# Kernel optimization log

Hardware: AMD Instinct MI355X
Metric: run time of the kernel (lower is better)

Reference implementation:

```python
import jax, jax.numpy as jnp
import numpy as np

T, B, H, L = 1024, 64, 512, 2


def setup_inputs() -> dict:
    key = jax.random.key(0)
    ks = jax.random.split(key, 5)
    s = 1.0 / np.sqrt(H)
    return {
        "x": jax.random.normal(ks[0], (T, B, H), jnp.float32),
        "h0": jnp.zeros((L, B, H), jnp.float32),
        "c0": jnp.zeros((L, B, H), jnp.float32),
        "W_ih": jax.random.uniform(ks[1], (L, 4 * H, H), jnp.float32, -s, s),
        "W_hh": jax.random.uniform(ks[2], (L, 4 * H, H), jnp.float32, -s, s),
        "b_ih": jax.random.uniform(ks[3], (L, 4 * H), jnp.float32, -s, s),
        "b_hh": jax.random.uniform(ks[4], (L, 4 * H), jnp.float32, -s, s),
    }


def _run_layer(x, h0, c0, W_ih, W_hh, b_ih, b_hh):
    # Precompute input-to-gate projections for all timesteps: [T, B, 4H]
    x_gates = jnp.einsum('tbi,gi->tbg', x, W_ih) + b_ih + b_hh

    def step(carry, xg):
        h, c = carry
        gates = xg + h @ W_hh.T  # [B, 4H]
        i, f, g, o = jnp.split(gates, 4, axis=-1)
        i = jax.nn.sigmoid(i)
        f = jax.nn.sigmoid(f)
        g = jnp.tanh(g)
        o = jax.nn.sigmoid(o)
        c_next = f * c + i * g
        h_next = o * jnp.tanh(c_next)
        return (h_next, c_next), h_next

    (h_n, c_n), out = jax.lax.scan(step, (h0, c0), x_gates)
    return out, h_n, c_n


def reference(x, h0, c0, W_ih, W_hh, b_ih, b_hh):
    h_ns, c_ns = [], []
    layer_out = x
    for l in range(L):
        layer_out, h_n, c_n = _run_layer(
            layer_out, h0[l], c0[l], W_ih[l], W_hh[l], b_ih[l], b_hh[l])
        h_ns.append(h_n)
        c_ns.append(c_n)
    return layer_out, jnp.stack(h_ns, 0), jnp.stack(c_ns, 0)
```

## Files before the change

kernel.cpp:

```cpp
#include <hip/hip_runtime.h>
#include <math.h>

#define TT 1024
#define BB 64
#define HH 512
#define G4 2048
#define NBLK 256
#define NTHR 1024
#define KH (HH * BB)

#define HN_OFF ((size_t)TT * BB * HH)
#define CN_OFF (HN_OFF + (size_t)2 * BB * HH)

__device__ inline float sigm(float v) {
    return 1.0f / (1.0f + __expf(-v));
}
__device__ inline float tanh_fast(float v) {
    const float e = __expf(2.0f * v);
    return 1.0f - 2.0f / (e + 1.0f);
}

__device__ inline void store_coh(float* p, float v) {
    __hip_atomic_store(p, v, __ATOMIC_RELAXED, __HIP_MEMORY_SCOPE_AGENT);
}

extern "C" __global__ void __launch_bounds__(256)
xpose(const float* __restrict__ x, float* __restrict__ xT)
{
    __shared__ float tile[64][65];
    const int t   = blockIdx.x;
    const int kc  = blockIdx.y << 6;
    const int tid = threadIdx.x;

    const int kk = tid & 63;
    const int b0 = tid >> 6;
    const float* xp = x + (size_t)t * BB * HH;
    #pragma unroll
    for (int i = 0; i < 16; ++i) {
        const int b = b0 + (i << 2);
        tile[b][kk] = xp[(size_t)b * HH + kc + kk];
    }
    __syncthreads();
    const int b  = tid & 63;
    const int k0 = tid >> 6;
    float* xo = xT + (size_t)t * KH + (size_t)kc * BB;
    #pragma unroll
    for (int i = 0; i < 16; ++i) {
        const int kl = k0 + (i << 2);
        xo[kl * BB + b] = tile[b][kl];
    }
}

__device__ inline void grid_barrier(unsigned* gbar, unsigned* groot,
                                    unsigned barIdx, int bid)
{
    __syncthreads();
    if (threadIdx.x == 0) {
        const int g = bid & 15;
        const unsigned old = __hip_atomic_fetch_add(
            &gbar[g * 16], 1u, __ATOMIC_RELAXED, __HIP_MEMORY_SCOPE_AGENT);
        if (old == barIdx * 16u + 15u) {
            __hip_atomic_fetch_add(groot, 1u, __ATOMIC_RELAXED,
                                   __HIP_MEMORY_SCOPE_AGENT);
        }
        const unsigned tgt = (barIdx + 1u) * 16u;
        while (__hip_atomic_load(groot, __ATOMIC_RELAXED,
                                 __HIP_MEMORY_SCOPE_AGENT) < tgt) {
            __builtin_amdgcn_s_sleep(1);
        }
        __builtin_amdgcn_fence(__ATOMIC_ACQUIRE, "agent");
    }
    __syncthreads();
}

extern "C" __global__ void __launch_bounds__(NTHR)
lstm_scan(const float* __restrict__ h0,
          const float* __restrict__ c0,
          const float* __restrict__ Wih,
          const float* __restrict__ Whh,
          const float* __restrict__ bih,
          const float* __restrict__ bhh,
          const float* __restrict__ xT,
          float* __restrict__ out,
          float* __restrict__ h0buf,
          float* __restrict__ h1buf,
          unsigned* __restrict__ gbar,
          unsigned* __restrict__ groot)
{
    __shared__ float red[16][8][64];
    __shared__ __align__(16) float wlds[16][8][128];

    const int tid  = threadIdx.x;
    const int lane = tid & 63;
    const int w    = __builtin_amdgcn_readfirstlane(tid >> 6);
    const int bid  = blockIdx.x;
    const int hk0  = bid << 1;

    const int kbase = (w & 3) << 7;
    const int grp   = w >> 2;

    const float* Wbase;
    if      (grp == 0) Wbase = Wih;
    else if (grp == 1) Wbase = Whh;
    else if (grp == 2) Wbase = Wih + (size_t)G4 * HH;
    else               Wbase = Whh + (size_t)G4 * HH;

    #pragma unroll
    for (int rr = 0; rr < 8; ++rr) {
        const int row = ((rr >> 1) << 9) + hk0 + (rr & 1);
        const float* src = Wbase + (size_t)row * HH + kbase;
        wlds[w][rr][lane]      = src[lane];
        wlds[w][rr][lane + 64] = src[lane + 64];
    }

    float creg[2] = {0.f, 0.f};
    float bs[8];
    if (w == 0) {
        #pragma unroll
        for (int u = 0; u < 2; ++u) {
            const int hk = hk0 + u;
            store_coh(&h0buf[hk * BB + lane], h0[(size_t)lane * HH + hk]);
            creg[u] = c0[(size_t)lane * HH + hk];
        }
        #pragma unroll
        for (int rr = 0; rr < 8; ++rr) {
            const int row = ((rr >> 1) << 9) + hk0 + (rr & 1);
            bs[rr] = bih[row] + bhh[row];
        }
    } else if (w == 1) {
        #pragma unroll
        for (int u = 0; u < 2; ++u) {
            const int hk = hk0 + u;
            store_coh(&h1buf[hk * BB + lane], h0[(size_t)(BB + lane) * HH + hk]);
            creg[u] = c0[(size_t)(BB + lane) * HH + hk];
        }
        #pragma unroll
        for (int rr = 0; rr < 8; ++rr) {
            const int row = ((rr >> 1) << 9) + hk0 + (rr & 1);
            bs[rr] = bih[G4 + row] + bhh[G4 + row];
        }
    }

    unsigned barIdx = 0;
    grid_barrier(gbar, groot, barIdx, bid); ++barIdx;

    const float* wl = &wlds[w][0][0];

    for (int s = 0; s <= TT; ++s) {
        const float* act;
        if (grp == 0) {
            const int t0 = (s < TT) ? s : (TT - 1);
            act = xT + (size_t)t0 * KH + (size_t)kbase * BB;
        } else if (grp <= 2) {
            act = h0buf + (size_t)(s & 1) * KH + (size_t)kbase * BB;
        } else {
            act = h1buf + (size_t)((s + 1) & 1) * KH + (size_t)kbase * BB;
        }

        float acc[8];
        #pragma unroll
        for (int rr = 0; rr < 8; ++rr) acc[rr] = 0.0f;

        #pragma unroll 2
        for (int j = 0; j < 128; j += 4) {
            const float a0 = act[(j + 0) * BB + lane];
            const float a1 = act[(j + 1) * BB + lane];
            const float a2 = act[(j + 2) * BB + lane];
            const float a3 = act[(j + 3) * BB + lane];
            #pragma unroll
            for (int rr = 0; rr < 8; ++rr) {
                const float4 wv = *(const float4*)(wl + rr * 128 + j);
                acc[rr] = fmaf(a3, wv.w,
                           fmaf(a2, wv.z,
                            fmaf(a1, wv.y,
                             fmaf(a0, wv.x, acc[rr]))));
            }
        }

        #pragma unroll
        for (int rr = 0; rr < 8; ++rr) red[w][rr][lane] = acc[rr];
        __syncthreads();

        if (w == 0) {
            if (s < TT) {
                float g[8];
                #pragma unroll
                for (int rr = 0; rr < 8; ++rr) {
                    float t = red[0][rr][lane] + red[1][rr][lane]
                            + red[2][rr][lane] + red[3][rr][lane]
                            + red[4][rr][lane] + red[5][rr][lane]
                            + red[6][rr][lane] + red[7][rr][lane];
                    g[rr] = bs[rr] + t;
                }
                #pragma unroll
                for (int u = 0; u < 2; ++u) {
                    const float ig = sigm(g[0 + u]);
                    const float fg = sigm(g[2 + u]);
                    const float gg = tanh_fast(g[4 + u]);
                    const float og = sigm(g[6 + u]);
                    const float cn = fg * creg[u] + ig * gg;
                    const float hn = og * tanh_fast(cn);
                    creg[u] = cn;
                    const int hk = hk0 + u;
                    store_coh(&h0buf[(size_t)((s + 1) & 1) * KH + hk * BB + lane], hn);
                    if (s == TT - 1) {
                        out[HN_OFF + (size_t)lane * HH + hk] = hn;
                        out[CN_OFF + (size_t)lane * HH + hk] = cn;
                    }
                }
            }
        } else if (w == 1) {
            if (s >= 1) {
                const int t1 = s - 1;
                float g[8];
                #pragma unroll
                for (int rr = 0; rr < 8; ++rr) {
                    float t = red[8][rr][lane]  + red[9][rr][lane]
                            + red[10][rr][lane] + red[11][rr][lane]
                            + red[12][rr][lane] + red[13][rr][lane]
                            + red[14][rr][lane] + red[15][rr][lane];
                    g[rr] = bs[rr] + t;
                }
                #pragma unroll
                for (int u = 0; u < 2; ++u) {
                    const float ig = sigm(g[0 + u]);
                    const float fg = sigm(g[2 + u]);
                    const float gg = tanh_fast(g[4 + u]);
                    const float og = sigm(g[6 + u]);
                    const float cn = fg * creg[u] + ig * gg;
                    const float hn = og * tanh_fast(cn);
                    creg[u] = cn;
                    const int hk = hk0 + u;
                    store_coh(&h1buf[(size_t)(s & 1) * KH + hk * BB + lane], hn);
                    out[(size_t)t1 * BB * HH + (size_t)lane * HH + hk] = hn;
                    if (t1 == TT - 1) {
                        out[HN_OFF + (size_t)(BB + lane) * HH + hk] = hn;
                        out[CN_OFF + (size_t)(BB + lane) * HH + hk] = cn;
                    }
                }
            }
        }
        grid_barrier(gbar, groot, barIdx, bid); ++barIdx;
    }
}

extern "C" void kernel_launch(void* const* d_in, const int* in_sizes, int n_in,
                              void* d_out, int out_size, void* d_ws, size_t ws_size,
                              hipStream_t stream)
{
    (void)in_sizes; (void)n_in; (void)out_size; (void)ws_size;
    const float* x   = (const float*)d_in[0];
    const float* h0  = (const float*)d_in[1];
    const float* c0  = (const float*)d_in[2];
    const float* Wih = (const float*)d_in[3];
    const float* Whh = (const float*)d_in[4];
    const float* bih = (const float*)d_in[5];
    const float* bhh = (const float*)d_in[6];
    float* out = (float*)d_out;

    float* xT    = (float*)d_ws;
    float* h0buf = xT + (size_t)TT * KH;
    float* h1buf = h0buf + (size_t)2 * KH;
    unsigned* gbar  = (unsigned*)(h1buf + (size_t)2 * KH);
    unsigned* groot = gbar + 256;

    hipMemsetAsync(gbar, 0, (256 + 64) * sizeof(unsigned), stream);

    xpose<<<dim3(TT, 8), 256, 0, stream>>>(x, xT);

    void* args[] = {(void*)&h0, (void*)&c0, (void*)&Wih, (void*)&Whh,
                    (void*)&bih, (void*)&bhh, (void*)&xT, (void*)&out,
                    (void*)&h0buf, (void*)&h1buf, (void*)&gbar, (void*)&groot};
    hipLaunchCooperativeKernel((void*)lstm_scan, dim3(NBLK), dim3(NTHR),
                               args, 0, stream);
}
```

Measured before the change: 17.70 ms.

## Retile inner dot product to packed 2-wide FMAs over batch pairs

Each lane now handles two batch columns and four gate rows instead of one batch column and eight rows. Activations are loaded as float2 and accumulated with packed 2-wide FMAs, which halves the LDS weight reads per FMA and enables packed FP32 math. It also remaps block IDs to spread hidden units across XCDs, adds an occupancy hint to launch bounds, and vectorizes the layer-1 output stores to float2. Risks are higher register pressure and changed cache locality from the new block mapping.

After: 21.61 ms. 22.1% more time.

```diff
diff --git a/kernel.cpp b/kernel.cpp
--- a/kernel.cpp
+++ b/kernel.cpp
@@ -11,6 +11,8 @@
 
 #define HN_OFF ((size_t)TT * BB * HH)
 #define CN_OFF (HN_OFF + (size_t)2 * BB * HH)
+
+typedef float v2f __attribute__((ext_vector_type(2)));
 
 __device__ inline float sigm(float v) {
     return 1.0f / (1.0f + __expf(-v));
@@ -73,7 +75,7 @@
     __syncthreads();
 }
 
-extern "C" __global__ void __launch_bounds__(NTHR)
+extern "C" __global__ void __launch_bounds__(NTHR, 4)
 lstm_scan(const float* __restrict__ h0,
           const float* __restrict__ c0,
           const float* __restrict__ Wih,
@@ -87,17 +89,21 @@
           unsigned* __restrict__ gbar,
           unsigned* __restrict__ groot)
 {
-    __shared__ float red[16][8][64];
+    __shared__ __align__(16) float red[16][8][64];
     __shared__ __align__(16) float wlds[16][8][128];
 
     const int tid  = threadIdx.x;
     const int lane = tid & 63;
     const int w    = __builtin_amdgcn_readfirstlane(tid >> 6);
     const int bid  = blockIdx.x;
-    const int hk0  = bid << 1;
+    const int vb   = ((bid & 7) << 5) | (bid >> 3);
+    const int hk0  = vb << 1;
 
     const int kbase = (w & 3) << 7;
     const int grp   = w >> 2;
+
+    const int rg = lane >> 5;
+    const int b0 = (lane & 31) << 1;
 
     const float* Wbase;
     if      (grp == 0) Wbase = Wih;
@@ -144,7 +150,7 @@
     unsigned barIdx = 0;
     grid_barrier(gbar, groot, barIdx, bid); ++barIdx;
 
-    const float* wl = &wlds[w][0][0];
+    const float* wl = &wlds[w][rg << 2][0];
 
     for (int s = 0; s <= TT; ++s) {
         const float* act;
@@ -156,29 +162,36 @@
         } else {
             act = h1buf + (size_t)((s + 1) & 1) * KH + (size_t)kbase * BB;
         }
-
-        float acc[8];
-        #pragma unroll
-        for (int rr = 0; rr < 8; ++rr) acc[rr] = 0.0f;
+        const float* actp = act + b0;
+
+        v2f acc2[4];
+        #pragma unroll
+        for (int q = 0; q < 4; ++q) acc2[q] = (v2f){0.f, 0.f};
 
         #pragma unroll 2
         for (int j = 0; j < 128; j += 4) {
-            const float a0 = act[(j + 0) * BB + lane];
-            const float a1 = act[(j + 1) * BB + lane];
-            const float a2 = act[(j + 2) * BB + lane];
-            const float a3 = act[(j + 3) * BB + lane];
+            const v2f a0 = *(const v2f*)(actp + (j + 0) * BB);
+            const v2f a1 = *(const v2f*)(actp + (j + 1) * BB);
+            const v2f a2 = *(const v2f*)(actp + (j + 2) * BB);
+            const v2f a3 = *(const v2f*)(actp + (j + 3) * BB);
             #pragma unroll
-            for (int rr = 0; rr < 8; ++rr) {
-                const float4 wv = *(const float4*)(wl + rr * 128 + j);
-                acc[rr] = fmaf(a3, wv.w,
-                           fmaf(a2, wv.z,
-                            fmaf(a1, wv.y,
-                             fmaf(a0, wv.x, acc[rr]))));
+            for (int q = 0; q < 4; ++q) {
+                const float4 wv = *(const float4*)(wl + q * 128 + j);
+                const v2f w0 = {wv.x, wv.x};
+                const v2f w1 = {wv.y, wv.y};
+                const v2f w2 = {wv.z, wv.z};
+                const v2f w3 = {wv.w, wv.w};
+                acc2[q] = __builtin_elementwise_fma(a0, w0, acc2[q]);
+                acc2[q] = __builtin_elementwise_fma(a1, w1, acc2[q]);
+                acc2[q] = __builtin_elementwise_fma(a2, w2, acc2[q]);
+                acc2[q] = __builtin_elementwise_fma(a3, w3, acc2[q]);
             }
         }
 
         #pragma unroll
-        for (int rr = 0; rr < 8; ++rr) red[w][rr][lane] = acc[rr];
+        for (int q = 0; q < 4; ++q) {
+            *(v2f*)&red[w][(rg << 2) + q][b0] = acc2[q];
+        }
         __syncthreads();
 
         if (w == 0) {
@@ -221,6 +234,7 @@
                             + red[14][rr][lane] + red[15][rr][lane];
                     g[rr] = bs[rr] + t;
                 }
+                float hn2[2], cn2[2];
                 #pragma unroll
                 for (int u = 0; u < 2; ++u) {
                     const float ig = sigm(g[0 + u]);
@@ -230,13 +244,17 @@
                     const float cn = fg * creg[u] + ig * gg;
                     const float hn = og * tanh_fast(cn);
                     creg[u] = cn;
+                    cn2[u] = cn; hn2[u] = hn;
                     const int hk = hk0 + u;
                     store_coh(&h1buf[(size_t)(s & 1) * KH + hk * BB + lane], hn);
-                    out[(size_t)t1 * BB * HH + (size_t)lane * HH + hk] = hn;
-                    if (t1 == TT - 1) {
-                        out[HN_OFF + (size_t)(BB + lane) * HH + hk] = hn;
-                        out[CN_OFF + (size_t)(BB + lane) * HH + hk] = cn;
-                    }
+                }
+                *(float2*)&out[(size_t)t1 * BB * HH + (size_t)lane * HH + hk0] =
+                    make_float2(hn2[0], hn2[1]);
+                if (t1 == TT - 1) {
+                    *(float2*)&out[HN_OFF + (size_t)(BB + lane) * HH + hk0] =
+                        make_float2(hn2[0], hn2[1]);
+                    *(float2*)&out[CN_OFF + (size_t)(BB + lane) * HH + hk0] =
+                        make_float2(cn2[0], cn2[1]);
                 }
             }
         }
```

## Use packed FMA accumulators, remap block IDs across XCDs, vectorize output stores

Applied to the files above, without the earlier changes.

Rewrites the inner dot-product to use 2-wide vector FMAs, so the compiler can emit packed FP32 FMA (v_pk_fma_f32) with two partial sums per row that are added at the end. It also permutes the block-to-hidden-unit mapping so that consecutive hidden pairs land on blocks spread over the XCDs, which may change L2 locality of the h buffers. Output h/c stores for the two hidden units are merged into float2 writes. Together these aim to cut FMA issue count and scattered store transactions inside the latency-bound recurrent loop. The changed summation order perturbs floating-point results slightly.

After: 14.99 ms. 15.3% less time.

```diff
diff --git a/kernel.cpp b/kernel.cpp
--- a/kernel.cpp
+++ b/kernel.cpp
@@ -11,6 +11,8 @@
 
 #define HN_OFF ((size_t)TT * BB * HH)
 #define CN_OFF (HN_OFF + (size_t)2 * BB * HH)
+
+typedef float v2f __attribute__((ext_vector_type(2)));
 
 __device__ inline float sigm(float v) {
     return 1.0f / (1.0f + __expf(-v));
@@ -87,14 +89,15 @@
           unsigned* __restrict__ gbar,
           unsigned* __restrict__ groot)
 {
-    __shared__ float red[16][8][64];
+    __shared__ __align__(16) float red[16][8][64];
     __shared__ __align__(16) float wlds[16][8][128];
 
     const int tid  = threadIdx.x;
     const int lane = tid & 63;
     const int w    = __builtin_amdgcn_readfirstlane(tid >> 6);
     const int bid  = blockIdx.x;
-    const int hk0  = bid << 1;
+    const int vb   = ((bid & 7) << 5) | (bid >> 3);
+    const int hk0  = vb << 1;
 
     const int kbase = (w & 3) << 7;
     const int grp   = w >> 2;
@@ -157,9 +160,9 @@
             act = h1buf + (size_t)((s + 1) & 1) * KH + (size_t)kbase * BB;
         }
 
-        float acc[8];
-        #pragma unroll
-        for (int rr = 0; rr < 8; ++rr) acc[rr] = 0.0f;
+        v2f acc2[8];
+        #pragma unroll
+        for (int rr = 0; rr < 8; ++rr) acc2[rr] = (v2f){0.f, 0.f};
 
         #pragma unroll 2
         for (int j = 0; j < 128; j += 4) {
@@ -167,18 +170,19 @@
             const float a1 = act[(j + 1) * BB + lane];
             const float a2 = act[(j + 2) * BB + lane];
             const float a3 = act[(j + 3) * BB + lane];
+            const v2f aA = {a0, a1};
+            const v2f aB = {a2, a3};
             #pragma unroll
             for (int rr = 0; rr < 8; ++rr) {
                 const float4 wv = *(const float4*)(wl + rr * 128 + j);
-                acc[rr] = fmaf(a3, wv.w,
-                           fmaf(a2, wv.z,
-                            fmaf(a1, wv.y,
-                             fmaf(a0, wv.x, acc[rr]))));
+                acc2[rr] = __builtin_elementwise_fma(aA, (v2f){wv.x, wv.y}, acc2[rr]);
+                acc2[rr] = __builtin_elementwise_fma(aB, (v2f){wv.z, wv.w}, acc2[rr]);
             }
         }
 
         #pragma unroll
-        for (int rr = 0; rr < 8; ++rr) red[w][rr][lane] = acc[rr];
+        for (int rr = 0; rr < 8; ++rr)
+            red[w][rr][lane] = acc2[rr].x + acc2[rr].y;
         __syncthreads();
 
         if (w == 0) {
@@ -192,6 +196,7 @@
                             + red[6][rr][lane] + red[7][rr][lane];
                     g[rr] = bs[rr] + t;
                 }
+                float hn2[2], cn2[2];
                 #pragma unroll
                 for (int u = 0; u < 2; ++u) {
                     const float ig = sigm(g[0 + u]);
@@ -201,12 +206,15 @@
                     const float cn = fg * creg[u] + ig * gg;
                     const float hn = og * tanh_fast(cn);
                     creg[u] = cn;
+                    cn2[u] = cn; hn2[u] = hn;
                     const int hk = hk0 + u;
                     store_coh(&h0buf[(size_t)((s + 1) & 1) * KH + hk * BB + lane], hn);
-                    if (s == TT - 1) {
-                        out[HN_OFF + (size_t)lane * HH + hk] = hn;
-                        out[CN_OFF + (size_t)lane * HH + hk] = cn;
-                    }
+                }
+                if (s == TT - 1) {
+                    *(float2*)&out[HN_OFF + (size_t)lane * HH + hk0] =
+                        make_float2(hn2[0], hn2[1]);
+                    *(float2*)&out[CN_OFF + (size_t)lane * HH + hk0] =
+                        make_float2(cn2[0], cn2[1]);
                 }
             }
         } else if (w == 1) {
@@ -221,6 +229,7 @@
                             + red[14][rr][lane] + red[15][rr][lane];
                     g[rr] = bs[rr] + t;
                 }
+                float hn2[2], cn2[2];
                 #pragma unroll
                 for (int u = 0; u < 2; ++u) {
                     const float ig = sigm(g[0 + u]);
@@ -230,13 +239,17 @@
                     const float cn = fg * creg[u] + ig * gg;
                     const float hn = og * tanh_fast(cn);
                     creg[u] = cn;
+                    cn2[u] = cn; hn2[u] = hn;
                     const int hk = hk0 + u;
                     store_coh(&h1buf[(size_t)(s & 1) * KH + hk * BB + lane], hn);
-                    out[(size_t)t1 * BB * HH + (size_t)lane * HH + hk] = hn;
-                    if (t1 == TT - 1) {
-                        out[HN_OFF + (size_t)(BB + lane) * HH + hk] = hn;
-                        out[CN_OFF + (size_t)(BB + lane) * HH + hk] = cn;
-                    }
+                }
+                *(float2*)&out[(size_t)t1 * BB * HH + (size_t)lane * HH + hk0] =
+                    make_float2(hn2[0], hn2[1]);
+                if (t1 == TT - 1) {
+                    *(float2*)&out[HN_OFF + (size_t)(BB + lane) * HH + hk0] =
+                        make_float2(hn2[0], hn2[1]);
+                    *(float2*)&out[CN_OFF + (size_t)(BB + lane) * HH + hk0] =
+                        make_float2(cn2[0], cn2[1]);
                 }
             }
         }
```
